# Kernel tuning notes

Hardware: AMD Instinct MI355X
Metric: run time of the kernel (lower is better)

## Reference

```python
import jax, jax.numpy as jnp
import numpy as np

B, L, D, H, E, K = 1, 512, 512, 512, 32, 2

def setup_inputs() -> dict:
    key = jax.random.key(0)
    ks = jax.random.split(key, 6)
    x = jax.random.normal(ks[0], (B, L, D), dtype=jnp.float32)
    router_scale = 1.0 + 0.02 * jax.random.normal(ks[1], (D,), dtype=jnp.float32)
    router_logits_w = 0.02 * jax.random.normal(ks[2], (D, E), dtype=jnp.float32)
    gating_einsum = 0.02 * jax.random.normal(ks[3], (E, 2, H, D), dtype=jnp.float32)
    linear_w = 0.02 * jax.random.normal(ks[4], (E, H, D), dtype=jnp.float32)
    per_expert_scale = 1.0 + 0.02 * jax.random.normal(ks[5], (E,), dtype=jnp.float32)
    return {"x": x, "router_scale": router_scale, "router_logits_w": router_logits_w,
            "gating_einsum": gating_einsum, "linear_w": linear_w,
            "per_expert_scale": per_expert_scale}

def reference(x, router_scale, router_logits_w, gating_einsum, linear_w, per_expert_scale):
    d = x.shape[-1]
    n_experts = router_logits_w.shape[-1]
    # RMSNorm without scale (fp32)
    x32 = x.astype(jnp.float32)
    var = jnp.mean(jnp.square(x32), axis=-1, keepdims=True)
    router_input = x32 * jax.lax.rsqrt(var + 1e-6)
    root_size = jax.lax.rsqrt(jnp.asarray(d, dtype=router_input.dtype))
    router_input = router_input * root_size * router_scale.astype(router_input.dtype)
    logits = jnp.dot(router_input, router_logits_w).astype(jnp.float32)  # [B,L,E]
    probs = jax.nn.softmax(logits, axis=-1)
    _, top_k_indices = jax.lax.top_k(logits, K)  # [B,L,K]
    indicator = jax.nn.one_hot(top_k_indices, n_experts, dtype=probs.dtype).sum(axis=-2)
    gate_weights = indicator * probs
    renorm = jnp.sum(gate_weights, axis=-1, keepdims=True)
    renorm = jnp.where(renorm > 0.0, renorm, 1.0)
    weights = probs / renorm
    top_k_weights = jnp.take_along_axis(weights, top_k_indices, axis=-1)  # [B,L,K]
    output = jnp.zeros_like(x)
    for ki in range(K):  # small fixed k; faithful to source's per-slot gather
        expert_idx = top_k_indices[:, :, ki]          # [B,L] int32
        expert_w = top_k_weights[:, :, ki]            # [B,L]
        gate_params = gating_einsum[expert_idx]       # [B,L,2,H,D] -- the big gather
        lin_params = linear_w[expert_idx]             # [B,L,H,D]
        escale = per_expert_scale[expert_idx]         # [B,L]
        gate_0 = jnp.einsum('bld,blhd->blh', x, gate_params[:, :, 0])
        gate_1 = jnp.einsum('bld,blhd->blh', x, gate_params[:, :, 1])
        activated = jax.nn.gelu(gate_0) * gate_1
        expert_out = jnp.einsum('blh,blhd->bld', activated, lin_params)
        output = output + expert_out * (escale * expert_w)[..., None]
    return output
```

## Files before the change

kernel.cpp:

```cpp
#include <hip/hip_runtime.h>
#include <hip/hip_bf16.h>
#include <math.h>

#define LTOK 512
#define DDIM 512
#define NEXP 32
#define HDIM 512

typedef __attribute__((ext_vector_type(8))) short short8;
typedef __attribute__((ext_vector_type(4))) float floatx4;

__device__ __forceinline__ unsigned bpack(float a, float b) {
    unsigned ua = __float_as_uint(a), ub = __float_as_uint(b);
    ua += 0x7FFFu + ((ua >> 16) & 1u);
    ub += 0x7FFFu + ((ub >> 16) & 1u);
    return (ua >> 16) | (ub & 0xFFFF0000u);
}

#define RAW_BARRIER() do { \
    asm volatile("s_waitcnt lgkmcnt(0)" ::: "memory"); \
    __builtin_amdgcn_s_barrier(); \
} while (0)


__global__ __launch_bounds__(256) void router_kernel(
    const float* __restrict__ x, const float* __restrict__ rs,
    const float* __restrict__ Wr, const float* __restrict__ pes,
    int* __restrict__ easgn, float* __restrict__ wts,
    short* __restrict__ xb, float* __restrict__ out)
{
    const int t = blockIdx.x;
    const int tid = threadIdx.x;
    const int lane = tid & 63;
    const int wv = tid >> 6;

    float xv[2];
    float ss = 0.f;
#pragma unroll
    for (int j = 0; j < 2; ++j) {
        xv[j] = x[t * DDIM + j * 256 + tid];
        ss += xv[j] * xv[j];
    }
#pragma unroll
    for (int j = 0; j < 2; ++j) {
        xb[t * DDIM + j * 256 + tid] = (short)(bpack(xv[j], 0.f) & 0xFFFFu);
        out[t * DDIM + j * 256 + tid] = 0.f;
    }

#pragma unroll
    for (int o = 32; o > 0; o >>= 1) ss += __shfl_xor(ss, o);
    __shared__ float sred[4];
    if (lane == 0) sred[wv] = ss;
    __syncthreads();
    ss = (sred[0] + sred[1]) + (sred[2] + sred[3]);
    const float var = ss * (1.0f / 512.0f);
    const float coef = rsqrtf(var + 1e-6f) * rsqrtf(512.0f);

    __shared__ float ri[DDIM];
#pragma unroll
    for (int j = 0; j < 2; ++j) {
        const int d = j * 256 + tid;
        ri[d] = xv[j] * coef * rs[d];
    }
    __syncthreads();

    const int e = tid & 31;
    const int seg = tid >> 5;
    const int dbeg = seg * 64;
    float l0 = 0.f, l1 = 0.f, l2 = 0.f, l3 = 0.f;
#pragma unroll 4
    for (int d = dbeg; d < dbeg + 64; d += 4) {
        l0 = fmaf(ri[d + 0], Wr[(d + 0) * NEXP + e], l0);
        l1 = fmaf(ri[d + 1], Wr[(d + 1) * NEXP + e], l1);
        l2 = fmaf(ri[d + 2], Wr[(d + 2) * NEXP + e], l2);
        l3 = fmaf(ri[d + 3], Wr[(d + 3) * NEXP + e], l3);
    }
    __shared__ float lpart[8][NEXP];
    lpart[seg][e] = (l0 + l1) + (l2 + l3);
    __syncthreads();

    __shared__ float lgs[NEXP];
    if (tid < NEXP) {
        float v = 0.f;
#pragma unroll
        for (int s = 0; s < 8; ++s) v += lpart[s][tid];
        lgs[tid] = v;
    }
    __syncthreads();

    if (tid == 0) {
        int i0 = 0; float m0 = lgs[0];
        for (int i = 1; i < NEXP; ++i) if (lgs[i] > m0) { m0 = lgs[i]; i0 = i; }
        int i1 = -1; float m1 = -1e30f;
        for (int i = 0; i < NEXP; ++i) if (i != i0 && lgs[i] > m1) { m1 = lgs[i]; i1 = i; }
        const float e1 = expf(m1 - m0);
        const float inv = 1.0f / (1.0f + e1);
        easgn[2 * t]     = i0;
        easgn[2 * t + 1] = i1;
        wts[2 * t]     = inv * pes[i0];
        wts[2 * t + 1] = e1 * inv * pes[i1];
    }
}

__global__ __launch_bounds__(256, 4) void gates_kernel(
    const short* __restrict__ xb, const float* __restrict__ G,
    const int* __restrict__ easgn, short* __restrict__ act)
{
    const int e  = blockIdx.y;
    const int h0 = blockIdx.x * 16;
    const int tid = threadIdx.x;
    const int wv   = tid >> 6;
    const int g    = wv & 1;
    const int kh   = wv >> 1;
    const int lane = tid & 63;
    const int n    = lane & 15;
    const int quad = lane >> 4;

    __shared__ float red[4][2][4][64];
    __shared__ int toks[LTOK];
    __shared__ int lcnt;

    const int4 eg = ((const int4*)easgn)[tid];

    const float* Gl = G + ((size_t)((e * 2 + g) * HDIM) + h0 + n) * DDIM + kh * 256 + quad * 8;
    floatx4 u0[8], u1[8];
#pragma unroll
    for (int ks = 0; ks < 8; ++ks) {
        u0[ks] = *(const floatx4*)(Gl + ks * 32);
        u1[ks] = *(const floatx4*)(Gl + ks * 32 + 4);
    }

    if (tid == 0) lcnt = 0;
    RAW_BARRIER();
    if (eg.x == e) { int p = atomicAdd(&lcnt, 1); toks[p] = 4 * tid; }
    if (eg.y == e) { int p = atomicAdd(&lcnt, 1); toks[p] = 4 * tid + 1; }
    if (eg.z == e) { int p = atomicAdd(&lcnt, 1); toks[p] = 4 * tid + 2; }
    if (eg.w == e) { int p = atomicAdd(&lcnt, 1); toks[p] = 4 * tid + 3; }
    RAW_BARRIER();
    const int Ne = lcnt;
    if (Ne == 0) return;

    short8 Bg[8];
#pragma unroll
    for (int ks = 0; ks < 8; ++ks) {
        union { short8 s; unsigned u[4]; } B;
        B.u[0] = bpack(u0[ks].x, u0[ks].y);
        B.u[1] = bpack(u0[ks].z, u0[ks].w);
        B.u[2] = bpack(u1[ks].x, u1[ks].y);
        B.u[3] = bpack(u1[ks].z, u1[ks].w);
        Bg[ks] = B.s;
    }

    const short* xbh = xb + kh * 256;

    for (int mb = 0; mb < Ne; mb += 32) {
        int arow[2];
#pragma unroll
        for (int i = 0; i < 2; ++i) {
            int s = mb + i * 16 + n;
            arow[i] = toks[s < Ne ? s : Ne - 1] >> 1;
        }
        floatx4 acc[2] = {};
#pragma unroll
        for (int ks = 0; ks < 8; ++ks) {
            const int ko = ks * 32 + quad * 8;
#pragma unroll
            for (int i = 0; i < 2; ++i) {
                const short8 A = *(const short8*)(xbh + (size_t)arow[i] * DDIM + ko);
                acc[i] = __builtin_amdgcn_mfma_f32_16x16x32_bf16(A, Bg[ks], acc[i], 0, 0, 0);
            }
        }
#pragma unroll
        for (int i = 0; i < 2; ++i)
#pragma unroll
            for (int r = 0; r < 4; ++r)
                red[wv][i][r][lane] = acc[i][r];
        __syncthreads();

        {
            const int i = wv & 1;
            const int u = wv >> 1;
#pragma unroll
            for (int rr = 0; rr < 2; ++rr) {
                const int r = u * 2 + rr;
                const int s = mb + i * 16 + quad * 4 + r;
                if (s < Ne) {
                    const int a = toks[s];
                    const float g0 = red[0][i][r][lane] + red[2][i][r][lane];
                    const float g1 = red[1][i][r][lane] + red[3][i][r][lane];
                    const float uu = 0.7978845608f * (g0 + 0.044715f * g0 * g0 * g0);
                    const float sg = 1.0f / (1.0f + __expf(-2.0f * uu));
                    const float v = g0 * sg * g1;
                    act[(size_t)a * HDIM + h0 + n] = (short)(bpack(v, 0.f) & 0xFFFFu);
                }
            }
        }
        __syncthreads();
    }
}

__global__ __launch_bounds__(256, 4) void linear_kernel(
    const short* __restrict__ act, const float* __restrict__ Wl,
    const int* __restrict__ easgn, const float* __restrict__ wts,
    float* __restrict__ out)
{
    const int e  = blockIdx.y;
    const int d0 = blockIdx.x * 16;
    const int tid = threadIdx.x;
    const int wv   = tid >> 6;
    const int lane = tid & 63;
    const int n    = lane & 15;
    const int quad = lane >> 4;

    __shared__ float red[4][2][4][64];
    __shared__ int   toks[LTOK];
    __shared__ float wsl[LTOK];
    __shared__ int   lcnt;

    const int4 eg = ((const int4*)easgn)[tid];
    const float4 wt4 = ((const float4*)wts)[tid];

    const float* Wbase = Wl + ((size_t)e * HDIM + wv * 128 + quad * 8) * DDIM + d0 + n;
    float w[32];
#pragma unroll
    for (int ks = 0; ks < 4; ++ks)
#pragma unroll
        for (int j = 0; j < 8; ++j)
            w[ks * 8 + j] = Wbase[(size_t)(ks * 32 + j) * DDIM];

    if (tid == 0) lcnt = 0;
    RAW_BARRIER();
    if (eg.x == e) { int p = atomicAdd(&lcnt, 1); toks[p] = 4 * tid;     wsl[p] = wt4.x; }
    if (eg.y == e) { int p = atomicAdd(&lcnt, 1); toks[p] = 4 * tid + 1; wsl[p] = wt4.y; }
    if (eg.z == e) { int p = atomicAdd(&lcnt, 1); toks[p] = 4 * tid + 2; wsl[p] = wt4.z; }
    if (eg.w == e) { int p = atomicAdd(&lcnt, 1); toks[p] = 4 * tid + 3; wsl[p] = wt4.w; }
    RAW_BARRIER();
    const int Ne = lcnt;
    if (Ne == 0) return;

    short8 Bl[4];
#pragma unroll
    for (int ks = 0; ks < 4; ++ks) {
        union { short8 s; unsigned u[4]; } B;
        B.u[0] = bpack(w[ks * 8 + 0], w[ks * 8 + 1]);
        B.u[1] = bpack(w[ks * 8 + 2], w[ks * 8 + 3]);
        B.u[2] = bpack(w[ks * 8 + 4], w[ks * 8 + 5]);
        B.u[3] = bpack(w[ks * 8 + 6], w[ks * 8 + 7]);
        Bl[ks] = B.s;
    }

    for (int mb = 0; mb < Ne; mb += 32) {
        int arow[2];
#pragma unroll
        for (int i = 0; i < 2; ++i) {
            int s = mb + i * 16 + n;
            arow[i] = toks[s < Ne ? s : Ne - 1];
        }
        floatx4 acc[2] = {};
#pragma unroll
        for (int ks = 0; ks < 4; ++ks) {
            const int ko = wv * 128 + ks * 32 + quad * 8;
#pragma unroll
            for (int i = 0; i < 2; ++i) {
                const short8 A = *(const short8*)(act + (size_t)arow[i] * HDIM + ko);
                acc[i] = __builtin_amdgcn_mfma_f32_16x16x32_bf16(A, Bl[ks], acc[i], 0, 0, 0);
            }
        }
#pragma unroll
        for (int i = 0; i < 2; ++i)
#pragma unroll
            for (int r = 0; r < 4; ++r)
                red[wv][i][r][lane] = acc[i][r];
        __syncthreads();

        {
            const int i = wv & 1;
            const int u = wv >> 1;
#pragma unroll
            for (int rr = 0; rr < 2; ++rr) {
                const int r = u * 2 + rr;
                const int s = mb + i * 16 + quad * 4 + r;
                if (s < Ne) {
                    const int slot = toks[s];
                    const float v = ((red[0][i][r][lane] + red[1][i][r][lane]) +
                                     (red[2][i][r][lane] + red[3][i][r][lane])) * wsl[s];
                    atomicAdd(&out[(size_t)(slot >> 1) * DDIM + d0 + n], v);
                }
            }
        }
        __syncthreads();
    }
}

extern "C" void kernel_launch(void* const* d_in, const int* in_sizes, int n_in,
                              void* d_out, int out_size, void* d_ws, size_t ws_size,
                              hipStream_t stream)
{
    const float* x   = (const float*)d_in[0];
    const float* rs  = (const float*)d_in[1];
    const float* Wr  = (const float*)d_in[2];
    const float* G   = (const float*)d_in[3];
    const float* Wl  = (const float*)d_in[4];
    const float* pes = (const float*)d_in[5];
    float* out = (float*)d_out;

    char* ws = (char*)d_ws;
    int*   easgn = (int*)(ws);
    float* wts   = (float*)(ws + 4096);
    short* xb    = (short*)(ws + 8192);
    short* act   = (short*)(ws + 532480);

    router_kernel<<<dim3(LTOK), dim3(256), 0, stream>>>(x, rs, Wr, pes, easgn, wts, xb, out);
    gates_kernel<<<dim3(32, NEXP), dim3(256), 0, stream>>>(xb, G, easgn, act);
    linear_kernel<<<dim3(32, NEXP), dim3(256), 0, stream>>>(act, Wl, easgn, wts, out);
}
```

Measured before the change: 151.6 us.

## Fuse router, gate and linear stages into one cooperative persistent kernel

Replaces the three separate launches with a single cooperative kernel of 1024 blocks that uses grid-wide syncs between the router, gate-projection and down-projection phases. Each block starts loading its expert weight tile before the router phase and before the second grid sync, so weight fetches overlap the earlier phases. This removes launch gaps and hides weight load latency. The cost is two grid barriers, more register pressure, and a requirement that all 1024 blocks fit on the device at once; if the cooperative launch fails, the old three-kernel path runs instead.

```diff
diff --git a/kernel.cpp b/kernel.cpp
--- a/kernel.cpp
+++ b/kernel.cpp
@@ -1,6 +1,9 @@
 #include <hip/hip_runtime.h>
 #include <hip/hip_bf16.h>
+#include <hip/hip_cooperative_groups.h>
 #include <math.h>
+
+namespace cg = cooperative_groups;
 
 #define LTOK 512
 #define DDIM 512
@@ -22,6 +25,250 @@
     __builtin_amdgcn_s_barrier(); \
 } while (0)
 
+
+__global__ __launch_bounds__(256, 4) void moe_fused(
+    const float* __restrict__ x, const float* __restrict__ rs,
+    const float* __restrict__ Wr, const float* __restrict__ pes,
+    const float* __restrict__ G, const float* __restrict__ Wl,
+    int* __restrict__ easgn, float* __restrict__ wts,
+    short* __restrict__ xb, short* __restrict__ act,
+    float* __restrict__ out)
+{
+    cg::grid_group gg = cg::this_grid();
+
+    const int bid  = blockIdx.x;
+    const int e    = bid >> 5;
+    const int tile = bid & 31;
+    const int tid  = threadIdx.x;
+    const int wv   = tid >> 6;
+    const int lane = tid & 63;
+    const int n    = lane & 15;
+    const int quad = lane >> 4;
+    const int g    = wv & 1;
+    const int kh   = wv >> 1;
+    const int h0   = tile * 16;
+    const int d0   = tile * 16;
+
+    __shared__ float red[4][2][4][64];
+    __shared__ int   toks[LTOK];
+    __shared__ float wsl[LTOK];
+    __shared__ int   lcnt;
+    __shared__ float ri[DDIM];
+    __shared__ float sred[4];
+    __shared__ float lpart[8][NEXP];
+    __shared__ float lgs[NEXP];
+
+    const float* Gl = G + ((size_t)((e * 2 + g) * HDIM) + h0 + n) * DDIM + kh * 256 + quad * 8;
+    floatx4 u0[8], u1[8];
+#pragma unroll
+    for (int ks = 0; ks < 8; ++ks) {
+        u0[ks] = *(const floatx4*)(Gl + ks * 32);
+        u1[ks] = *(const floatx4*)(Gl + ks * 32 + 4);
+    }
+
+    if (bid < LTOK) {
+        const int t = bid;
+        float xv[2];
+        float ss = 0.f;
+#pragma unroll
+        for (int j = 0; j < 2; ++j) {
+            xv[j] = x[t * DDIM + j * 256 + tid];
+            ss += xv[j] * xv[j];
+        }
+#pragma unroll
+        for (int j = 0; j < 2; ++j) {
+            xb[t * DDIM + j * 256 + tid] = (short)(bpack(xv[j], 0.f) & 0xFFFFu);
+            out[t * DDIM + j * 256 + tid] = 0.f;
+        }
+
+#pragma unroll
+        for (int o = 32; o > 0; o >>= 1) ss += __shfl_xor(ss, o);
+        if (lane == 0) sred[wv] = ss;
+        __syncthreads();
+        ss = (sred[0] + sred[1]) + (sred[2] + sred[3]);
+        const float var = ss * (1.0f / 512.0f);
+        const float coef = rsqrtf(var + 1e-6f) * rsqrtf(512.0f);
+
+#pragma unroll
+        for (int j = 0; j < 2; ++j) {
+            const int d = j * 256 + tid;
+            ri[d] = xv[j] * coef * rs[d];
+        }
+        __syncthreads();
+
+        const int er  = tid & 31;
+        const int seg = tid >> 5;
+        const int dbeg = seg * 64;
+        float l0 = 0.f, l1 = 0.f, l2 = 0.f, l3 = 0.f;
+#pragma unroll 4
+        for (int d = dbeg; d < dbeg + 64; d += 4) {
+            l0 = fmaf(ri[d + 0], Wr[(d + 0) * NEXP + er], l0);
+            l1 = fmaf(ri[d + 1], Wr[(d + 1) * NEXP + er], l1);
+            l2 = fmaf(ri[d + 2], Wr[(d + 2) * NEXP + er], l2);
+            l3 = fmaf(ri[d + 3], Wr[(d + 3) * NEXP + er], l3);
+        }
+        lpart[seg][er] = (l0 + l1) + (l2 + l3);
+        __syncthreads();
+
+        if (tid < NEXP) {
+            float v = 0.f;
+#pragma unroll
+            for (int s = 0; s < 8; ++s) v += lpart[s][tid];
+            lgs[tid] = v;
+        }
+        __syncthreads();
+
+        if (tid == 0) {
+            int i0 = 0; float m0 = lgs[0];
+            for (int i = 1; i < NEXP; ++i) if (lgs[i] > m0) { m0 = lgs[i]; i0 = i; }
+            int i1 = -1; float m1 = -1e30f;
+            for (int i = 0; i < NEXP; ++i) if (i != i0 && lgs[i] > m1) { m1 = lgs[i]; i1 = i; }
+            const float e1 = expf(m1 - m0);
+            const float inv = 1.0f / (1.0f + e1);
+            easgn[2 * t]     = i0;
+            easgn[2 * t + 1] = i1;
+            wts[2 * t]     = inv * pes[i0];
+            wts[2 * t + 1] = e1 * inv * pes[i1];
+        }
+    }
+
+    gg.sync();
+
+    const int4  eg  = ((const int4*)easgn)[tid];
+    const float4 wt4 = ((const float4*)wts)[tid];
+    if (tid == 0) lcnt = 0;
+    __syncthreads();
+    if (eg.x == e) { int p = atomicAdd(&lcnt, 1); toks[p] = 4 * tid;     wsl[p] = wt4.x; }
+    if (eg.y == e) { int p = atomicAdd(&lcnt, 1); toks[p] = 4 * tid + 1; wsl[p] = wt4.y; }
+    if (eg.z == e) { int p = atomicAdd(&lcnt, 1); toks[p] = 4 * tid + 2; wsl[p] = wt4.z; }
+    if (eg.w == e) { int p = atomicAdd(&lcnt, 1); toks[p] = 4 * tid + 3; wsl[p] = wt4.w; }
+    __syncthreads();
+    const int Ne = lcnt;
+
+    short8 Bg[8];
+#pragma unroll
+    for (int ks = 0; ks < 8; ++ks) {
+        union { short8 s; unsigned u[4]; } B;
+        B.u[0] = bpack(u0[ks].x, u0[ks].y);
+        B.u[1] = bpack(u0[ks].z, u0[ks].w);
+        B.u[2] = bpack(u1[ks].x, u1[ks].y);
+        B.u[3] = bpack(u1[ks].z, u1[ks].w);
+        Bg[ks] = B.s;
+    }
+
+    if (Ne > 0) {
+        const short* xbh = xb + kh * 256;
+        for (int mb = 0; mb < Ne; mb += 32) {
+            int arow[2];
+#pragma unroll
+            for (int i = 0; i < 2; ++i) {
+                int s = mb + i * 16 + n;
+                arow[i] = toks[s < Ne ? s : Ne - 1] >> 1;
+            }
+            floatx4 acc[2] = {};
+#pragma unroll
+            for (int ks = 0; ks < 8; ++ks) {
+                const int ko = ks * 32 + quad * 8;
+#pragma unroll
+                for (int i = 0; i < 2; ++i) {
+                    const short8 A = *(const short8*)(xbh + (size_t)arow[i] * DDIM + ko);
+                    acc[i] = __builtin_amdgcn_mfma_f32_16x16x32_bf16(A, Bg[ks], acc[i], 0, 0, 0);
+                }
+            }
+#pragma unroll
+            for (int i = 0; i < 2; ++i)
+#pragma unroll
+                for (int r = 0; r < 4; ++r)
+                    red[wv][i][r][lane] = acc[i][r];
+            __syncthreads();
+
+            {
+                const int i = wv & 1;
+                const int u = wv >> 1;
+#pragma unroll
+                for (int rr = 0; rr < 2; ++rr) {
+                    const int r = u * 2 + rr;
+                    const int s = mb + i * 16 + quad * 4 + r;
+                    if (s < Ne) {
+                        const int a = toks[s];
+                        const float g0 = red[0][i][r][lane] + red[2][i][r][lane];
+                        const float g1 = red[1][i][r][lane] + red[3][i][r][lane];
+                        const float uu = 0.7978845608f * (g0 + 0.044715f * g0 * g0 * g0);
+                        const float sg = 1.0f / (1.0f + __expf(-2.0f * uu));
+                        const float v = g0 * sg * g1;
+                        act[(size_t)a * HDIM + h0 + n] = (short)(bpack(v, 0.f) & 0xFFFFu);
+                    }
+                }
+            }
+            __syncthreads();
+        }
+    }
+
+    const float* Wbase = Wl + ((size_t)e * HDIM + wv * 128 + quad * 8) * DDIM + d0 + n;
+    float w[32];
+#pragma unroll
+    for (int ks = 0; ks < 4; ++ks)
+#pragma unroll
+        for (int j = 0; j < 8; ++j)
+            w[ks * 8 + j] = Wbase[(size_t)(ks * 32 + j) * DDIM];
+
+    gg.sync();
+
+    short8 Bl[4];
+#pragma unroll
+    for (int ks = 0; ks < 4; ++ks) {
+        union { short8 s; unsigned u[4]; } B;
+        B.u[0] = bpack(w[ks * 8 + 0], w[ks * 8 + 1]);
+        B.u[1] = bpack(w[ks * 8 + 2], w[ks * 8 + 3]);
+        B.u[2] = bpack(w[ks * 8 + 4], w[ks * 8 + 5]);
+        B.u[3] = bpack(w[ks * 8 + 6], w[ks * 8 + 7]);
+        Bl[ks] = B.s;
+    }
+
+    if (Ne > 0) {
+        for (int mb = 0; mb < Ne; mb += 32) {
+            int arow[2];
+#pragma unroll
+            for (int i = 0; i < 2; ++i) {
+                int s = mb + i * 16 + n;
+                arow[i] = toks[s < Ne ? s : Ne - 1];
+            }
+            floatx4 acc[2] = {};
+#pragma unroll
+            for (int ks = 0; ks < 4; ++ks) {
+                const int ko = wv * 128 + ks * 32 + quad * 8;
+#pragma unroll
+                for (int i = 0; i < 2; ++i) {
+                    const short8 A = *(const short8*)(act + (size_t)arow[i] * HDIM + ko);
+                    acc[i] = __builtin_amdgcn_mfma_f32_16x16x32_bf16(A, Bl[ks], acc[i], 0, 0, 0);
+                }
+            }
+#pragma unroll
+            for (int i = 0; i < 2; ++i)
+#pragma unroll
+                for (int r = 0; r < 4; ++r)
+                    red[wv][i][r][lane] = acc[i][r];
+            __syncthreads();
+
+            {
+                const int i = wv & 1;
+                const int u = wv >> 1;
+#pragma unroll
+                for (int rr = 0; rr < 2; ++rr) {
+                    const int r = u * 2 + rr;
+                    const int s = mb + i * 16 + quad * 4 + r;
+                    if (s < Ne) {
+                        const int slot = toks[s];
+                        const float v = ((red[0][i][r][lane] + red[1][i][r][lane]) +
+                                         (red[2][i][r][lane] + red[3][i][r][lane])) * wsl[s];
+                        atomicAdd(&out[(size_t)(slot >> 1) * DDIM + d0 + n], v);
+                    }
+                }
+            }
+            __syncthreads();
+        }
+    }
+}
 
 __global__ __launch_bounds__(256) void router_kernel(
     const float* __restrict__ x, const float* __restrict__ rs,
@@ -310,7 +557,16 @@
     short* xb    = (short*)(ws + 8192);
     short* act   = (short*)(ws + 532480);
 
-    router_kernel<<<dim3(LTOK), dim3(256), 0, stream>>>(x, rs, Wr, pes, easgn, wts, xb, out);
-    gates_kernel<<<dim3(32, NEXP), dim3(256), 0, stream>>>(xb, G, easgn, act);
-    linear_kernel<<<dim3(32, NEXP), dim3(256), 0, stream>>>(act, Wl, easgn, wts, out);
+    void* args[] = {
+        (void*)&x, (void*)&rs, (void*)&Wr, (void*)&pes, (void*)&G, (void*)&Wl,
+        (void*)&easgn, (void*)&wts, (void*)&xb, (void*)&act, (void*)&out
+    };
+    hipError_t err = hipLaunchCooperativeKernel(
+        (const void*)moe_fused, dim3(1024), dim3(256), args, 0, stream);
+
+    if (err != hipSuccess) {
+        router_kernel<<<dim3(LTOK), dim3(256), 0, stream>>>(x, rs, Wr, pes, easgn, wts, xb, out);
+        gates_kernel<<<dim3(32, NEXP), dim3(256), 0, stream>>>(xb, G, easgn, act);
+        linear_kernel<<<dim3(32, NEXP), dim3(256), 0, stream>>>(act, Wl, easgn, wts, out);
+    }
 }
```

Result: slower. 405.7 us (+167.6%).

## Fuse gates and linear kernels with per-expert atomic completion counters

Applied to the files above, without the earlier changes.

Merges the gate-projection and linear-projection kernels into a single expert kernel. Each block computes its slice of activations, signals a per-expert counter, then spins until all 32 tiles of that expert finish before running the linear projection. This removes one kernel launch and its drain/fill gap, and lets the linear weight loads overlap with other blocks' gate work. In exchange it relies on all blocks of an expert being co-resident; 1024 blocks at 4 per CU should fit on the device, but deadlock is possible if they do not.

```diff
diff --git a/kernel.cpp b/kernel.cpp
--- a/kernel.cpp
+++ b/kernel.cpp
@@ -27,12 +27,15 @@
     const float* __restrict__ x, const float* __restrict__ rs,
     const float* __restrict__ Wr, const float* __restrict__ pes,
     int* __restrict__ easgn, float* __restrict__ wts,
-    short* __restrict__ xb, float* __restrict__ out)
+    short* __restrict__ xb, float* __restrict__ out,
+    int* __restrict__ done)
 {
     const int t = blockIdx.x;
     const int tid = threadIdx.x;
     const int lane = tid & 63;
     const int wv = tid >> 6;
+
+    if (t == 0 && tid < NEXP) done[tid] = 0;
 
     float xv[2];
     float ss = 0.f;
@@ -102,13 +105,18 @@
     }
 }
 
-__global__ __launch_bounds__(256, 4) void gates_kernel(
+__global__ __launch_bounds__(256, 4) void expert_kernel(
     const short* __restrict__ xb, const float* __restrict__ G,
-    const int* __restrict__ easgn, short* __restrict__ act)
+    const float* __restrict__ Wl,
+    const int* __restrict__ easgn, const float* __restrict__ wts,
+    short* __restrict__ act, float* __restrict__ out,
+    int* __restrict__ done)
 {
-    const int e  = blockIdx.y;
-    const int h0 = blockIdx.x * 16;
-    const int tid = threadIdx.x;
+    const int e    = blockIdx.y;
+    const int tile = blockIdx.x;
+    const int h0   = tile * 16;
+    const int d0   = tile * 16;
+    const int tid  = threadIdx.x;
     const int wv   = tid >> 6;
     const int g    = wv & 1;
     const int kh   = wv >> 1;
@@ -117,10 +125,12 @@
     const int quad = lane >> 4;
 
     __shared__ float red[4][2][4][64];
-    __shared__ int toks[LTOK];
-    __shared__ int lcnt;
-
-    const int4 eg = ((const int4*)easgn)[tid];
+    __shared__ int   toks[LTOK];
+    __shared__ float wsl[LTOK];
+    __shared__ int   lcnt;
+
+    const int4   eg  = ((const int4*)easgn)[tid];
+    const float4 wt4 = ((const float4*)wts)[tid];
 
     const float* Gl = G + ((size_t)((e * 2 + g) * HDIM) + h0 + n) * DDIM + kh * 256 + quad * 8;
     floatx4 u0[8], u1[8];
@@ -129,104 +139,6 @@
         u0[ks] = *(const floatx4*)(Gl + ks * 32);
         u1[ks] = *(const floatx4*)(Gl + ks * 32 + 4);
     }
-
-    if (tid == 0) lcnt = 0;
-    RAW_BARRIER();
-    if (eg.x == e) { int p = atomicAdd(&lcnt, 1); toks[p] = 4 * tid; }
-    if (eg.y == e) { int p = atomicAdd(&lcnt, 1); toks[p] = 4 * tid + 1; }
-    if (eg.z == e) { int p = atomicAdd(&lcnt, 1); toks[p] = 4 * tid + 2; }
-    if (eg.w == e) { int p = atomicAdd(&lcnt, 1); toks[p] = 4 * tid + 3; }
-    RAW_BARRIER();
-    const int Ne = lcnt;
-    if (Ne == 0) return;
-
-    short8 Bg[8];
-#pragma unroll
-    for (int ks = 0; ks < 8; ++ks) {
-        union { short8 s; unsigned u[4]; } B;
-        B.u[0] = bpack(u0[ks].x, u0[ks].y);
-        B.u[1] = bpack(u0[ks].z, u0[ks].w);
-        B.u[2] = bpack(u1[ks].x, u1[ks].y);
-        B.u[3] = bpack(u1[ks].z, u1[ks].w);
-        Bg[ks] = B.s;
-    }
-
-    const short* xbh = xb + kh * 256;
-
-    for (int mb = 0; mb < Ne; mb += 32) {
-        int arow[2];
-#pragma unroll
-        for (int i = 0; i < 2; ++i) {
-            int s = mb + i * 16 + n;
-            arow[i] = toks[s < Ne ? s : Ne - 1] >> 1;
-        }
-        floatx4 acc[2] = {};
-#pragma unroll
-        for (int ks = 0; ks < 8; ++ks) {
-            const int ko = ks * 32 + quad * 8;
-#pragma unroll
-            for (int i = 0; i < 2; ++i) {
-                const short8 A = *(const short8*)(xbh + (size_t)arow[i] * DDIM + ko);
-                acc[i] = __builtin_amdgcn_mfma_f32_16x16x32_bf16(A, Bg[ks], acc[i], 0, 0, 0);
-            }
-        }
-#pragma unroll
-        for (int i = 0; i < 2; ++i)
-#pragma unroll
-            for (int r = 0; r < 4; ++r)
-                red[wv][i][r][lane] = acc[i][r];
-        __syncthreads();
-
-        {
-            const int i = wv & 1;
-            const int u = wv >> 1;
-#pragma unroll
-            for (int rr = 0; rr < 2; ++rr) {
-                const int r = u * 2 + rr;
-                const int s = mb + i * 16 + quad * 4 + r;
-                if (s < Ne) {
-                    const int a = toks[s];
-                    const float g0 = red[0][i][r][lane] + red[2][i][r][lane];
-                    const float g1 = red[1][i][r][lane] + red[3][i][r][lane];
-                    const float uu = 0.7978845608f * (g0 + 0.044715f * g0 * g0 * g0);
-                    const float sg = 1.0f / (1.0f + __expf(-2.0f * uu));
-                    const float v = g0 * sg * g1;
-                    act[(size_t)a * HDIM + h0 + n] = (short)(bpack(v, 0.f) & 0xFFFFu);
-                }
-            }
-        }
-        __syncthreads();
-    }
-}
-
-__global__ __launch_bounds__(256, 4) void linear_kernel(
-    const short* __restrict__ act, const float* __restrict__ Wl,
-    const int* __restrict__ easgn, const float* __restrict__ wts,
-    float* __restrict__ out)
-{
-    const int e  = blockIdx.y;
-    const int d0 = blockIdx.x * 16;
-    const int tid = threadIdx.x;
-    const int wv   = tid >> 6;
-    const int lane = tid & 63;
-    const int n    = lane & 15;
-    const int quad = lane >> 4;
-
-    __shared__ float red[4][2][4][64];
-    __shared__ int   toks[LTOK];
-    __shared__ float wsl[LTOK];
-    __shared__ int   lcnt;
-
-    const int4 eg = ((const int4*)easgn)[tid];
-    const float4 wt4 = ((const float4*)wts)[tid];
-
-    const float* Wbase = Wl + ((size_t)e * HDIM + wv * 128 + quad * 8) * DDIM + d0 + n;
-    float w[32];
-#pragma unroll
-    for (int ks = 0; ks < 4; ++ks)
-#pragma unroll
-        for (int j = 0; j < 8; ++j)
-            w[ks * 8 + j] = Wbase[(size_t)(ks * 32 + j) * DDIM];
 
     if (tid == 0) lcnt = 0;
     RAW_BARRIER();
@@ -236,7 +148,87 @@
     if (eg.w == e) { int p = atomicAdd(&lcnt, 1); toks[p] = 4 * tid + 3; wsl[p] = wt4.w; }
     RAW_BARRIER();
     const int Ne = lcnt;
+
+    short8 Bg[8];
+#pragma unroll
+    for (int ks = 0; ks < 8; ++ks) {
+        union { short8 s; unsigned u[4]; } B;
+        B.u[0] = bpack(u0[ks].x, u0[ks].y);
+        B.u[1] = bpack(u0[ks].z, u0[ks].w);
+        B.u[2] = bpack(u1[ks].x, u1[ks].y);
+        B.u[3] = bpack(u1[ks].z, u1[ks].w);
+        Bg[ks] = B.s;
+    }
+
+    if (Ne > 0) {
+        const short* xbh = xb + kh * 256;
+        for (int mb = 0; mb < Ne; mb += 32) {
+            int arow[2];
+#pragma unroll
+            for (int i = 0; i < 2; ++i) {
+                int s = mb + i * 16 + n;
+                arow[i] = toks[s < Ne ? s : Ne - 1] >> 1;
+            }
+            floatx4 acc[2] = {};
+#pragma unroll
+            for (int ks = 0; ks < 8; ++ks) {
+                const int ko = ks * 32 + quad * 8;
+#pragma unroll
+                for (int i = 0; i < 2; ++i) {
+                    const short8 A = *(const short8*)(xbh + (size_t)arow[i] * DDIM + ko);
+                    acc[i] = __builtin_amdgcn_mfma_f32_16x16x32_bf16(A, Bg[ks], acc[i], 0, 0, 0);
+                }
+            }
+#pragma unroll
+            for (int i = 0; i < 2; ++i)
+#pragma unroll
+                for (int r = 0; r < 4; ++r)
+                    red[wv][i][r][lane] = acc[i][r];
+            __syncthreads();
+
+            {
+                const int i = wv & 1;
+                const int u = wv >> 1;
+#pragma unroll
+                for (int rr = 0; rr < 2; ++rr) {
+                    const int r = u * 2 + rr;
+                    const int s = mb + i * 16 + quad * 4 + r;
+                    if (s < Ne) {
+                        const int a = toks[s];
+                        const float g0 = red[0][i][r][lane] + red[2][i][r][lane];
+                        const float g1 = red[1][i][r][lane] + red[3][i][r][lane];
+                        const float uu = 0.7978845608f * (g0 + 0.044715f * g0 * g0 * g0);
+                        const float sg = 1.0f / (1.0f + __expf(-2.0f * uu));
+                        const float v = g0 * sg * g1;
+                        act[(size_t)a * HDIM + h0 + n] = (short)(bpack(v, 0.f) & 0xFFFFu);
+                    }
+                }
+            }
+            __syncthreads();
+        }
+    }
+
+    __threadfence();
+    __syncthreads();
+    if (tid == 0)
+        __hip_atomic_fetch_add(&done[e], 1, __ATOMIC_RELEASE, __HIP_MEMORY_SCOPE_AGENT);
+
     if (Ne == 0) return;
+
+    const float* Wbase = Wl + ((size_t)e * HDIM + wv * 128 + quad * 8) * DDIM + d0 + n;
+    float w[32];
+#pragma unroll
+    for (int ks = 0; ks < 4; ++ks)
+#pragma unroll
+        for (int j = 0; j < 8; ++j)
+            w[ks * 8 + j] = Wbase[(size_t)(ks * 32 + j) * DDIM];
+
+    if (tid == 0) {
+        while (__hip_atomic_load(&done[e], __ATOMIC_ACQUIRE, __HIP_MEMORY_SCOPE_AGENT) < NEXP)
+            __builtin_amdgcn_s_sleep(8);
+    }
+    __syncthreads();
+    (void)__hip_atomic_load(&done[e], __ATOMIC_ACQUIRE, __HIP_MEMORY_SCOPE_AGENT);
 
     short8 Bl[4];
 #pragma unroll
@@ -309,8 +301,8 @@
     float* wts   = (float*)(ws + 4096);
     short* xb    = (short*)(ws + 8192);
     short* act   = (short*)(ws + 532480);
-
-    router_kernel<<<dim3(LTOK), dim3(256), 0, stream>>>(x, rs, Wr, pes, easgn, wts, xb, out);
-    gates_kernel<<<dim3(32, NEXP), dim3(256), 0, stream>>>(xb, G, easgn, act);
-    linear_kernel<<<dim3(32, NEXP), dim3(256), 0, stream>>>(act, Wl, easgn, wts, out);
+    int*   done  = (int*)(ws + 1581056);
+
+    router_kernel<<<dim3(LTOK), dim3(256), 0, stream>>>(x, rs, Wr, pes, easgn, wts, xb, out, done);
+    expert_kernel<<<dim3(32, NEXP), dim3(256), 0, stream>>>(xb, G, Wl, easgn, wts, act, out, done);
 }
```

Measured after the change: 374.5 us. 147% more time.
